# Kernel tuning notes

Measured on AMD Instinct MI355X. Metric: run time of the kernel, lower is better.

The kernel has to match this reference:

```python
import jax, jax.numpy as jnp
import numpy as np

B, S, H, E, K = 4, 4096, 1024, 8, 2
DFF = 4 * H


def setup_inputs() -> dict:
    key = jax.random.key(0)
    ks = jax.random.split(key, 6)
    s_in = 1.0 / np.sqrt(H)
    s_ff = 1.0 / np.sqrt(DFF)
    return {
        "x": jax.random.normal(ks[0], (B, S, H), dtype=jnp.float32),
        "router_w": jax.random.normal(ks[1], (E, H), dtype=jnp.float32) * s_in,
        "router_b": jnp.zeros((E,), dtype=jnp.float32),
        "fc1_w": jax.random.normal(ks[2], (E, DFF, H), dtype=jnp.float32) * s_in,
        "fc1_b": jnp.zeros((E, DFF), dtype=jnp.float32),
        "fc2_w": jax.random.normal(ks[3], (E, H, DFF), dtype=jnp.float32) * s_ff,
        "fc2_b": jnp.zeros((E, H), dtype=jnp.float32),
    }


def reference(x, router_w, router_b, fc1_w, fc1_b, fc2_w, fc2_b):
    b, s, h = x.shape
    e = router_w.shape[0]
    k = K
    # Router: [B,S,E]
    logits = jnp.einsum("bsh,eh->bse", x, router_w) + router_b
    top_v, top_i = jax.lax.top_k(logits, k)            # [B,S,K]
    probs = jax.nn.softmax(top_v, axis=-1)             # softmax over top-k logits
    # Combine weights per expert [B,S,E]; top-k indices are distinct per token,
    # so summing one-hot*prob over k matches the original's gather-of-first-match.
    combine = jnp.sum(jax.nn.one_hot(top_i, e, dtype=x.dtype) * probs[..., None], axis=-2)
    xf = x.reshape(-1, h)            # [T,H], T = B*S
    cf = combine.reshape(-1, e)      # [T,E]
    out = jnp.zeros_like(xf)
    for ei in range(e):              # fixed small loop over experts
        hdn = jax.nn.relu(xf @ fc1_w[ei].T + fc1_b[ei])   # [T,4H]
        y = hdn @ fc2_w[ei].T + fc2_b[ei]                 # [T,H]
        out = out + cf[:, ei:ei + 1] * y                  # zero weight == not routed
    return out.reshape(b, s, h)
```

## Files before the change

### kernel.cpp

```cpp
#include <hip/hip_runtime.h>
#include <stdint.h>

#define T_TOKENS 16384
#define H_DIM 1024
#define E_NUM 8
#define DFF_DIM 4096

#define BMT 128
#define BNT 128
#define BKT 64
#define MT_CAP 264
#define PAD_ROWS (MT_CAP * BMT)
#define NCHUNK 4
#define MT_PER_CHUNK (MT_CAP / NCHUNK)
#define CHUNK_ROWS (MT_PER_CHUNK * BMT)

#define WS_COUNTS     0
#define WS_CURSOR     32
#define WS_OFFS       64
#define WS_SLOT_TOK   256
#define WS_SLOT_W     135424
#define WS_EIDX       270592
#define WS_EW         401664
#define WS_WC1        532736
#define WS_WC2        67641600
#define WS_XB         134750464
#define WS_HDN        168304896
#define WS_REQUIRED   237510912UL
#define WS_SMALL_ZERO 270592

typedef __attribute__((ext_vector_type(8))) short short8;
typedef __attribute__((ext_vector_type(4))) float f32x4;

__device__ __forceinline__ unsigned short f2bf(float f) {
  union { float f; unsigned int u; } v; v.f = f;
  unsigned int r = v.u + 0x7FFFu + ((v.u >> 16) & 1u);
  return (unsigned short)(r >> 16);
}

__device__ __forceinline__ void load_lds16(const void* g, void* l) {
  __builtin_amdgcn_global_load_lds(
      (const __attribute__((address_space(1))) void*)g,
      (__attribute__((address_space(3))) void*)l, 16, 0, 0);
}

__global__ void convert_weights(const float* __restrict__ w1,
                                const float* __restrict__ w2,
                                unsigned short* __restrict__ wc1,
                                unsigned short* __restrict__ wc2) {
  int i = blockIdx.x * blockDim.x + threadIdx.x;
  const float4* s1 = (const float4*)w1;
  const float4* s2 = (const float4*)w2;
  float4 a = s1[i];
  float4 b = s2[i];
  ushort4 ua, ub;
  ua.x = f2bf(a.x); ua.y = f2bf(a.y); ua.z = f2bf(a.z); ua.w = f2bf(a.w);
  ub.x = f2bf(b.x); ub.y = f2bf(b.y); ub.z = f2bf(b.z); ub.w = f2bf(b.w);
  ((ushort4*)wc1)[i] = ua;
  ((ushort4*)wc2)[i] = ub;
}

__global__ __launch_bounds__(256) void router_kernel(
    const float* __restrict__ x, const float* __restrict__ rw,
    const float* __restrict__ rb, unsigned short* __restrict__ xb,
    int* __restrict__ eidx, float* __restrict__ ew) {
  __shared__ float4 rws[E_NUM * 256];
  const int tid = threadIdx.x;
#pragma unroll
  for (int k = 0; k < 8; ++k) rws[k * 256 + tid] = ((const float4*)rw)[k * 256 + tid];
  __syncthreads();

  const int wave = tid >> 6;
  const int lane = tid & 63;
#pragma unroll
  for (int i = 0; i < 4; ++i) {
    const int t = blockIdx.x * 16 + wave * 4 + i;
    const float4* xrow = (const float4*)(x + (size_t)t * H_DIM);
    float4 xv[4];
#pragma unroll
    for (int j = 0; j < 4; ++j) xv[j] = xrow[j * 64 + lane];

    ushort4* xbrow = (ushort4*)(xb + (size_t)t * H_DIM);
#pragma unroll
    for (int j = 0; j < 4; ++j) {
      ushort4 o;
      o.x = f2bf(xv[j].x); o.y = f2bf(xv[j].y);
      o.z = f2bf(xv[j].z); o.w = f2bf(xv[j].w);
      xbrow[j * 64 + lane] = o;
    }

    float s[E_NUM];
#pragma unroll
    for (int e = 0; e < E_NUM; ++e) {
      float a = 0.f;
#pragma unroll
      for (int j = 0; j < 4; ++j) {
        float4 wv = rws[e * 256 + j * 64 + lane];
        a += xv[j].x * wv.x + xv[j].y * wv.y + xv[j].z * wv.z + xv[j].w * wv.w;
      }
      s[e] = a;
    }
#pragma unroll
    for (int off = 32; off; off >>= 1) {
#pragma unroll
      for (int e = 0; e < E_NUM; ++e) s[e] += __shfl_xor(s[e], off);
    }
    if (lane == 0) {
      float lg[E_NUM];
#pragma unroll
      for (int e = 0; e < E_NUM; ++e) lg[e] = s[e] + rb[e];
      int i0 = 0; float m0 = lg[0];
#pragma unroll
      for (int e = 1; e < E_NUM; ++e)
        if (lg[e] > m0) { m0 = lg[e]; i0 = e; }
      int i1 = -1; float m1 = -3.4e38f;
#pragma unroll
      for (int e = 0; e < E_NUM; ++e)
        if (e != i0 && lg[e] > m1) { m1 = lg[e]; i1 = e; }
      float e1 = expf(m1 - m0);
      float denom = 1.f + e1;
      ((int2*)eidx)[t] = make_int2(i0, i1);
      ((float2*)ew)[t] = make_float2(1.f / denom, e1 / denom);
    }
  }
}

__global__ __launch_bounds__(1024) void count_kernel(const int* __restrict__ eidx,
                                                     int* __restrict__ counts,
                                                     int* __restrict__ offs,
                                                     int* __restrict__ cursor) {
  __shared__ int hist[E_NUM];
  const int tid = threadIdx.x;
  const int lane = tid & 63;
  if (tid < E_NUM) hist[tid] = 0;
  __syncthreads();
  int c[E_NUM];
#pragma unroll
  for (int e = 0; e < E_NUM; ++e) c[e] = 0;
  const int4* p = (const int4*)eidx;
#pragma unroll
  for (int i = 0; i < 8; ++i) {
    int4 v = p[i * 1024 + tid];
#pragma unroll
    for (int e = 0; e < E_NUM; ++e)
      c[e] += (v.x == e) + (v.y == e) + (v.z == e) + (v.w == e);
  }
#pragma unroll
  for (int off = 32; off; off >>= 1) {
#pragma unroll
    for (int e = 0; e < E_NUM; ++e) c[e] += __shfl_xor(c[e], off);
  }
  if (lane == 0) {
#pragma unroll
    for (int e = 0; e < E_NUM; ++e) atomicAdd(&hist[e], c[e]);
  }
  __syncthreads();
  if (tid == 0) {
    int acc = 0;
    offs[0] = 0;
#pragma unroll
    for (int e = 0; e < E_NUM; ++e) {
      counts[e] = hist[e];
      cursor[e] = 0;
      acc += ((hist[e] + BMT - 1) / BMT) * BMT;
      offs[e + 1] = acc;
    }
  }
}

__global__ __launch_bounds__(1024) void scatter_kernel(
    const int* __restrict__ eidx, const float* __restrict__ ew,
    const int* __restrict__ offs, int* __restrict__ cursor,
    int* __restrict__ slot_token, float* __restrict__ slot_w) {
  __shared__ int wcnt[16][E_NUM];
  __shared__ int wpre[16][E_NUM];
  __shared__ int bbase[E_NUM];
  __shared__ int soffs[E_NUM];
  const int tid = threadIdx.x, w = tid >> 6, lane = tid & 63;
  const int t = blockIdx.x * 1024 + tid;
  const int2 epair = ((const int2*)eidx)[t];
  const float2 wpair = ((const float2*)ew)[t];
  const int e0 = epair.x, e1 = epair.y;
  const unsigned long long lt = (1ULL << lane) - 1ULL;
  if (tid < E_NUM) soffs[tid] = offs[tid];
  int r0 = 0, r1 = 0;
#pragma unroll
  for (int e = 0; e < E_NUM; ++e) {
    unsigned long long m0 = __ballot(e0 == e);
    unsigned long long m1 = __ballot(e1 == e);
    int c0 = __popcll(m0);
    if (e0 == e) r0 = __popcll(m0 & lt);
    if (e1 == e) r1 = c0 + __popcll(m1 & lt);
    if (lane == 0) wcnt[w][e] = c0 + __popcll(m1);
  }
  __syncthreads();
  if (tid < E_NUM) {
    int run = 0;
#pragma unroll
    for (int w2 = 0; w2 < 16; ++w2) {
      wpre[w2][tid] = run;
      run += wcnt[w2][tid];
    }
    bbase[tid] = atomicAdd(&cursor[tid], run);
  }
  __syncthreads();
  const int s0 = soffs[e0] + bbase[e0] + wpre[w][e0] + r0;
  slot_token[s0] = t;
  slot_w[s0] = wpair.x;
  const int s1 = soffs[e1] + bbase[e1] + wpre[w][e1] + r1;
  slot_token[s1] = t;
  slot_w[s1] = wpair.y;
}

template <int KTOT>
__device__ __forceinline__ void gemm_core(const unsigned short* const* aptr,
                                          const unsigned short* const* bptr,
                                          unsigned short* lA, unsigned short* lB,
                                          f32x4 acc[4][4]) {
  const int tid = threadIdx.x;
  const int w = tid >> 6, lane = tid & 63;
  const int wm = w >> 1, wn = w & 1;
  const int rrow = lane & 15;
  const int rq = lane >> 4;

  for (int ks = 0; ks < KTOT / BKT; ++ks) {
    const int k0 = ks * BKT;
#pragma unroll
    for (int i = 0; i < 4; ++i) {
      load_lds16(aptr[i] + k0, lA + (i * 32 + w * 8) * BKT);
      load_lds16(bptr[i] + k0, lB + (i * 32 + w * 8) * BKT);
    }
    __syncthreads();
#pragma unroll
    for (int kk = 0; kk < 2; ++kk) {
      short8 af[4], bfr[4];
#pragma unroll
      for (int mi = 0; mi < 4; ++mi)
        af[mi] = *(const short8*)(lA + (wm * 64 + mi * 16 + rrow) * BKT + kk * 32 + rq * 8);
#pragma unroll
      for (int ni = 0; ni < 4; ++ni)
        bfr[ni] = *(const short8*)(lB + (wn * 64 + ni * 16 + rrow) * BKT + kk * 32 + rq * 8);
#pragma unroll
      for (int mi = 0; mi < 4; ++mi)
#pragma unroll
        for (int ni = 0; ni < 4; ++ni)
          acc[mi][ni] = __builtin_amdgcn_mfma_f32_16x16x32_bf16(af[mi], bfr[ni], acc[mi][ni], 0, 0, 0);
    }
    __syncthreads();
  }
}

__global__ __launch_bounds__(256, 2) void fc1_kernel(
    const unsigned short* __restrict__ xb, const unsigned short* __restrict__ wc1,
    const float* __restrict__ fc1_b, const int* __restrict__ offs,
    const int* __restrict__ counts, const int* __restrict__ slot_token,
    unsigned short* __restrict__ hdn, int chunk) {
  __shared__ unsigned short sA[BMT * BKT];
  __shared__ unsigned short sB[BNT * BKT];
  const int mt = chunk * MT_PER_CHUNK + blockIdx.y;
  const int row0 = mt * BMT;
  if (row0 >= offs[E_NUM]) return;
  int e = 0;
#pragma unroll
  for (int i = 1; i < E_NUM; ++i) e = (row0 >= offs[i]) ? i : e;
  const int n0 = blockIdx.x * BNT;

  f32x4 acc[4][4];
  f32x4 zf = {0.f, 0.f, 0.f, 0.f};
#pragma unroll
  for (int mi = 0; mi < 4; ++mi)
#pragma unroll
    for (int ni = 0; ni < 4; ++ni) acc[mi][ni] = zf;

  const int w = threadIdx.x >> 6;
  const int lane = threadIdx.x & 63;
  const int srow = w * 8 + (lane >> 3);
  const int scol = (lane & 7) * 8;
  const unsigned short* Bm = wc1 + (size_t)e * DFF_DIM * H_DIM + (size_t)n0 * H_DIM;
  const unsigned short* aptr[4];
  const unsigned short* bptr[4];
#pragma unroll
  for (int i = 0; i < 4; ++i) {
    const int r = i * 32 + srow;
    const int tok = slot_token[row0 + r];
    aptr[i] = xb + (size_t)tok * H_DIM + scol;
    bptr[i] = Bm + (size_t)r * H_DIM + scol;
  }
  gemm_core<H_DIM>(aptr, bptr, sA, sB, acc);

  const int wm = w >> 1, wn = w & 1;
  const int rrow = lane & 15, rq = lane >> 4;
  const int cnt = counts[e];
  const int lbase = row0 - offs[e];
  const int hrow0 = row0 - chunk * CHUNK_ROWS;
#pragma unroll
  for (int mi = 0; mi < 4; ++mi) {
#pragma unroll
    for (int j = 0; j < 4; ++j) {
      const int rit = wm * 64 + mi * 16 + rq * 4 + j;
      if (lbase + rit >= cnt) continue;
      unsigned short* hrow = hdn + (size_t)(hrow0 + rit) * DFF_DIM;
#pragma unroll
      for (int ni = 0; ni < 4; ++ni) {
        const int n = n0 + wn * 64 + ni * 16 + rrow;
        float v = acc[mi][ni][j] + fc1_b[e * DFF_DIM + n];
        v = v > 0.f ? v : 0.f;
        hrow[n] = f2bf(v);
      }
    }
  }
}

__global__ __launch_bounds__(256, 2) void fc2_kernel(
    const unsigned short* __restrict__ hdn, const unsigned short* __restrict__ wc2,
    const float* __restrict__ fc2_b, const int* __restrict__ offs,
    const int* __restrict__ counts, const int* __restrict__ slot_token,
    const float* __restrict__ slot_w, float* __restrict__ out, int chunk) {
  __shared__ unsigned short sA[BMT * BKT];
  __shared__ unsigned short sB[BNT * BKT];
  const int mt = chunk * MT_PER_CHUNK + blockIdx.y;
  const int row0 = mt * BMT;
  if (row0 >= offs[E_NUM]) return;
  int e = 0;
#pragma unroll
  for (int i = 1; i < E_NUM; ++i) e = (row0 >= offs[i]) ? i : e;
  const int n0 = blockIdx.x * BNT;

  f32x4 acc[4][4];
  f32x4 zf = {0.f, 0.f, 0.f, 0.f};
#pragma unroll
  for (int mi = 0; mi < 4; ++mi)
#pragma unroll
    for (int ni = 0; ni < 4; ++ni) acc[mi][ni] = zf;

  const int w = threadIdx.x >> 6;
  const int lane = threadIdx.x & 63;
  const int srow = w * 8 + (lane >> 3);
  const int scol = (lane & 7) * 8;
  const unsigned short* A = hdn + (size_t)(blockIdx.y * BMT) * DFF_DIM;
  const unsigned short* Bm = wc2 + (size_t)e * H_DIM * DFF_DIM + (size_t)n0 * DFF_DIM;
  const unsigned short* aptr[4];
  const unsigned short* bptr[4];
#pragma unroll
  for (int i = 0; i < 4; ++i) {
    const int r = i * 32 + srow;
    aptr[i] = A + (size_t)r * DFF_DIM + scol;
    bptr[i] = Bm + (size_t)r * DFF_DIM + scol;
  }
  gemm_core<DFF_DIM>(aptr, bptr, sA, sB, acc);

  const int wm = w >> 1, wn = w & 1;
  const int rrow = lane & 15, rq = lane >> 4;
  const int cnt = counts[e];
#pragma unroll
  for (int mi = 0; mi < 4; ++mi) {
#pragma unroll
    for (int j = 0; j < 4; ++j) {
      const int rit = wm * 64 + mi * 16 + rq * 4 + j;
      const int gr = row0 + rit;
      if (gr - offs[e] >= cnt) continue;
      const int tok = slot_token[gr];
      const float wgt = slot_w[gr];
      float* orow = out + (size_t)tok * H_DIM;
#pragma unroll
      for (int ni = 0; ni < 4; ++ni) {
        const int h = n0 + wn * 64 + ni * 16 + rrow;
        float v = (acc[mi][ni][j] + fc2_b[e * H_DIM + h]) * wgt;
        atomicAdd(orow + h, v);
      }
    }
  }
}

extern "C" void kernel_launch(void* const* d_in, const int* in_sizes, int n_in,
                              void* d_out, int out_size, void* d_ws, size_t ws_size,
                              hipStream_t stream) {
  const float* x        = (const float*)d_in[0];
  const float* router_w = (const float*)d_in[1];
  const float* router_b = (const float*)d_in[2];
  const float* fc1_w    = (const float*)d_in[3];
  const float* fc1_b    = (const float*)d_in[4];
  const float* fc2_w    = (const float*)d_in[5];
  const float* fc2_b    = (const float*)d_in[6];
  float* out = (float*)d_out;

  char* ws = (char*)d_ws;
  int* counts            = (int*)(ws + WS_COUNTS);
  int* cursor            = (int*)(ws + WS_CURSOR);
  int* offs              = (int*)(ws + WS_OFFS);
  int* slot_token        = (int*)(ws + WS_SLOT_TOK);
  float* slot_w          = (float*)(ws + WS_SLOT_W);
  int* eidx              = (int*)(ws + WS_EIDX);
  float* ew              = (float*)(ws + WS_EW);
  unsigned short* wc1    = (unsigned short*)(ws + WS_WC1);
  unsigned short* wc2    = (unsigned short*)(ws + WS_WC2);
  unsigned short* xb     = (unsigned short*)(ws + WS_XB);
  unsigned short* hdn    = (unsigned short*)(ws + WS_HDN);

  hipMemsetAsync(d_out, 0, (size_t)T_TOKENS * H_DIM * sizeof(float), stream);
  if (ws_size < WS_REQUIRED) return;
  hipMemsetAsync(ws, 0, WS_SMALL_ZERO, stream);

  convert_weights<<<32768, 256, 0, stream>>>(fc1_w, fc2_w, wc1, wc2);
  router_kernel<<<T_TOKENS / 16, 256, 0, stream>>>(x, router_w, router_b, xb, eidx, ew);
  count_kernel<<<1, 1024, 0, stream>>>(eidx, counts, offs, cursor);
  scatter_kernel<<<T_TOKENS / 1024, 1024, 0, stream>>>(eidx, ew, offs, cursor, slot_token, slot_w);

  for (int c = 0; c < NCHUNK; ++c) {
    fc1_kernel<<<dim3(DFF_DIM / BNT, MT_PER_CHUNK), 256, 0, stream>>>(
        xb, wc1, fc1_b, offs, counts, slot_token, hdn, c);
    fc2_kernel<<<dim3(H_DIM / BNT, MT_PER_CHUNK), 256, 0, stream>>>(
        hdn, wc2, fc2_b, offs, counts, slot_token, slot_w, out, c);
  }
}
```

Baseline: 1.143 ms.

## Replace fc2 atomic scatter with bf16 slot outputs and a gather combine kernel

```diff
diff --git a/kernel.cpp b/kernel.cpp
--- a/kernel.cpp
+++ b/kernel.cpp
@@ -8,10 +8,9 @@
 
 #define BMT 128
 #define BNT 128
-#define BKT 64
 #define MT_CAP 264
 #define PAD_ROWS (MT_CAP * BMT)
-#define NCHUNK 4
+#define NCHUNK 8
 #define MT_PER_CHUNK (MT_CAP / NCHUNK)
 #define CHUNK_ROWS (MT_PER_CHUNK * BMT)
 
@@ -19,14 +18,15 @@
 #define WS_CURSOR     32
 #define WS_OFFS       64
 #define WS_SLOT_TOK   256
-#define WS_SLOT_W     135424
 #define WS_EIDX       270592
 #define WS_EW         401664
-#define WS_WC1        532736
-#define WS_WC2        67641600
-#define WS_XB         134750464
-#define WS_HDN        168304896
-#define WS_REQUIRED   237510912UL
+#define WS_TOKSLOT    532736
+#define WS_WC1        663808
+#define WS_WC2        67772672
+#define WS_XB         134881536
+#define WS_HDN        168435968
+#define WS_Y          203038976
+#define WS_REQUIRED   272244992UL
 #define WS_SMALL_ZERO 270592
 
 typedef __attribute__((ext_vector_type(8))) short short8;
@@ -36,6 +36,11 @@
   union { float f; unsigned int u; } v; v.f = f;
   unsigned int r = v.u + 0x7FFFu + ((v.u >> 16) & 1u);
   return (unsigned short)(r >> 16);
+}
+
+__device__ __forceinline__ float bf2f(unsigned short b) {
+  union { unsigned int u; float f; } v; v.u = ((unsigned int)b) << 16;
+  return v.f;
 }
 
 __device__ __forceinline__ void load_lds16(const void* g, void* l) {
@@ -169,9 +174,9 @@
 }
 
 __global__ __launch_bounds__(1024) void scatter_kernel(
-    const int* __restrict__ eidx, const float* __restrict__ ew,
-    const int* __restrict__ offs, int* __restrict__ cursor,
-    int* __restrict__ slot_token, float* __restrict__ slot_w) {
+    const int* __restrict__ eidx, const int* __restrict__ offs,
+    int* __restrict__ cursor, int* __restrict__ slot_token,
+    int* __restrict__ tokslot) {
   __shared__ int wcnt[16][E_NUM];
   __shared__ int wpre[16][E_NUM];
   __shared__ int bbase[E_NUM];
@@ -179,7 +184,6 @@
   const int tid = threadIdx.x, w = tid >> 6, lane = tid & 63;
   const int t = blockIdx.x * 1024 + tid;
   const int2 epair = ((const int2*)eidx)[t];
-  const float2 wpair = ((const float2*)ew)[t];
   const int e0 = epair.x, e1 = epair.y;
   const unsigned long long lt = (1ULL << lane) - 1ULL;
   if (tid < E_NUM) soffs[tid] = offs[tid];
@@ -205,14 +209,13 @@
   }
   __syncthreads();
   const int s0 = soffs[e0] + bbase[e0] + wpre[w][e0] + r0;
+  const int s1 = soffs[e1] + bbase[e1] + wpre[w][e1] + r1;
   slot_token[s0] = t;
-  slot_w[s0] = wpair.x;
-  const int s1 = soffs[e1] + bbase[e1] + wpre[w][e1] + r1;
   slot_token[s1] = t;
-  slot_w[s1] = wpair.y;
-}
-
-template <int KTOT>
+  ((int2*)tokslot)[t] = make_int2(s0, s1);
+}
+
+template <int KTOT, int BK, int NLD>
 __device__ __forceinline__ void gemm_core(const unsigned short* const* aptr,
                                           const unsigned short* const* bptr,
                                           unsigned short* lA, unsigned short* lB,
@@ -223,23 +226,23 @@
   const int rrow = lane & 15;
   const int rq = lane >> 4;
 
-  for (int ks = 0; ks < KTOT / BKT; ++ks) {
-    const int k0 = ks * BKT;
-#pragma unroll
-    for (int i = 0; i < 4; ++i) {
-      load_lds16(aptr[i] + k0, lA + (i * 32 + w * 8) * BKT);
-      load_lds16(bptr[i] + k0, lB + (i * 32 + w * 8) * BKT);
+  for (int ks = 0; ks < KTOT / BK; ++ks) {
+    const int k0 = ks * BK;
+#pragma unroll
+    for (int i = 0; i < NLD; ++i) {
+      load_lds16(aptr[i] + k0, lA + i * 2048 + w * 512);
+      load_lds16(bptr[i] + k0, lB + i * 2048 + w * 512);
     }
     __syncthreads();
 #pragma unroll
-    for (int kk = 0; kk < 2; ++kk) {
+    for (int kk = 0; kk < BK / 32; ++kk) {
       short8 af[4], bfr[4];
 #pragma unroll
       for (int mi = 0; mi < 4; ++mi)
-        af[mi] = *(const short8*)(lA + (wm * 64 + mi * 16 + rrow) * BKT + kk * 32 + rq * 8);
+        af[mi] = *(const short8*)(lA + (wm * 64 + mi * 16 + rrow) * BK + kk * 32 + rq * 8);
 #pragma unroll
       for (int ni = 0; ni < 4; ++ni)
-        bfr[ni] = *(const short8*)(lB + (wn * 64 + ni * 16 + rrow) * BKT + kk * 32 + rq * 8);
+        bfr[ni] = *(const short8*)(lB + (wn * 64 + ni * 16 + rrow) * BK + kk * 32 + rq * 8);
 #pragma unroll
       for (int mi = 0; mi < 4; ++mi)
 #pragma unroll
@@ -255,8 +258,8 @@
     const float* __restrict__ fc1_b, const int* __restrict__ offs,
     const int* __restrict__ counts, const int* __restrict__ slot_token,
     unsigned short* __restrict__ hdn, int chunk) {
-  __shared__ unsigned short sA[BMT * BKT];
-  __shared__ unsigned short sB[BNT * BKT];
+  __shared__ unsigned short sA[BMT * 64];
+  __shared__ unsigned short sB[BNT * 64];
   const int mt = chunk * MT_PER_CHUNK + blockIdx.y;
   const int row0 = mt * BMT;
   if (row0 >= offs[E_NUM]) return;
@@ -272,10 +275,9 @@
 #pragma unroll
     for (int ni = 0; ni < 4; ++ni) acc[mi][ni] = zf;
 
-  const int w = threadIdx.x >> 6;
-  const int lane = threadIdx.x & 63;
-  const int srow = w * 8 + (lane >> 3);
-  const int scol = (lane & 7) * 8;
+  const int tid = threadIdx.x;
+  const int srow = tid >> 3;
+  const int scol = (tid & 7) * 8;
   const unsigned short* Bm = wc1 + (size_t)e * DFF_DIM * H_DIM + (size_t)n0 * H_DIM;
   const unsigned short* aptr[4];
   const unsigned short* bptr[4];
@@ -286,8 +288,10 @@
     aptr[i] = xb + (size_t)tok * H_DIM + scol;
     bptr[i] = Bm + (size_t)r * H_DIM + scol;
   }
-  gemm_core<H_DIM>(aptr, bptr, sA, sB, acc);
-
+  gemm_core<H_DIM, 64, 4>(aptr, bptr, sA, sB, acc);
+
+  const int w = tid >> 6;
+  const int lane = tid & 63;
   const int wm = w >> 1, wn = w & 1;
   const int rrow = lane & 15, rq = lane >> 4;
   const int cnt = counts[e];
@@ -314,17 +318,17 @@
 __global__ __launch_bounds__(256, 2) void fc2_kernel(
     const unsigned short* __restrict__ hdn, const unsigned short* __restrict__ wc2,
     const float* __restrict__ fc2_b, const int* __restrict__ offs,
-    const int* __restrict__ counts, const int* __restrict__ slot_token,
-    const float* __restrict__ slot_w, float* __restrict__ out, int chunk) {
-  __shared__ unsigned short sA[BMT * BKT];
-  __shared__ unsigned short sB[BNT * BKT];
-  const int mt = chunk * MT_PER_CHUNK + blockIdx.y;
+    const int* __restrict__ counts, unsigned short* __restrict__ y, int chunk) {
+  __shared__ unsigned short sA[BMT * 128];
+  __shared__ unsigned short sB[BNT * 128];
+  const int mt_local = blockIdx.x >> 3;
+  const int mt = chunk * MT_PER_CHUNK + mt_local;
   const int row0 = mt * BMT;
   if (row0 >= offs[E_NUM]) return;
   int e = 0;
 #pragma unroll
   for (int i = 1; i < E_NUM; ++i) e = (row0 >= offs[i]) ? i : e;
-  const int n0 = blockIdx.x * BNT;
+  const int n0 = (blockIdx.x & 7) * BNT;
 
   f32x4 acc[4][4];
   f32x4 zf = {0.f, 0.f, 0.f, 0.f};
@@ -333,42 +337,65 @@
 #pragma unroll
     for (int ni = 0; ni < 4; ++ni) acc[mi][ni] = zf;
 
-  const int w = threadIdx.x >> 6;
-  const int lane = threadIdx.x & 63;
-  const int srow = w * 8 + (lane >> 3);
-  const int scol = (lane & 7) * 8;
-  const unsigned short* A = hdn + (size_t)(blockIdx.y * BMT) * DFF_DIM;
+  const int tid = threadIdx.x;
+  const int srow = tid >> 4;
+  const int scol = (tid & 15) * 8;
+  const unsigned short* A = hdn + (size_t)(mt_local * BMT) * DFF_DIM;
   const unsigned short* Bm = wc2 + (size_t)e * H_DIM * DFF_DIM + (size_t)n0 * DFF_DIM;
-  const unsigned short* aptr[4];
-  const unsigned short* bptr[4];
-#pragma unroll
-  for (int i = 0; i < 4; ++i) {
-    const int r = i * 32 + srow;
+  const unsigned short* aptr[8];
+  const unsigned short* bptr[8];
+#pragma unroll
+  for (int i = 0; i < 8; ++i) {
+    const int r = i * 16 + srow;
     aptr[i] = A + (size_t)r * DFF_DIM + scol;
     bptr[i] = Bm + (size_t)r * DFF_DIM + scol;
   }
-  gemm_core<DFF_DIM>(aptr, bptr, sA, sB, acc);
-
+  gemm_core<DFF_DIM, 128, 8>(aptr, bptr, sA, sB, acc);
+
+  const int w = tid >> 6;
+  const int lane = tid & 63;
   const int wm = w >> 1, wn = w & 1;
   const int rrow = lane & 15, rq = lane >> 4;
   const int cnt = counts[e];
+  const int lbase = row0 - offs[e];
 #pragma unroll
   for (int mi = 0; mi < 4; ++mi) {
 #pragma unroll
     for (int j = 0; j < 4; ++j) {
       const int rit = wm * 64 + mi * 16 + rq * 4 + j;
-      const int gr = row0 + rit;
-      if (gr - offs[e] >= cnt) continue;
-      const int tok = slot_token[gr];
-      const float wgt = slot_w[gr];
-      float* orow = out + (size_t)tok * H_DIM;
+      if (lbase + rit >= cnt) continue;
+      unsigned short* yrow = y + (size_t)(row0 + rit) * H_DIM;
 #pragma unroll
       for (int ni = 0; ni < 4; ++ni) {
         const int h = n0 + wn * 64 + ni * 16 + rrow;
-        float v = (acc[mi][ni][j] + fc2_b[e * H_DIM + h]) * wgt;
-        atomicAdd(orow + h, v);
+        yrow[h] = f2bf(acc[mi][ni][j] + fc2_b[e * H_DIM + h]);
       }
     }
+  }
+}
+
+__global__ __launch_bounds__(256) void combine_kernel(
+    const unsigned short* __restrict__ y, const int* __restrict__ tokslot,
+    const float* __restrict__ ew, float* __restrict__ out) {
+  const int wave = threadIdx.x >> 6;
+  const int lane = threadIdx.x & 63;
+  const int t = blockIdx.x * 4 + wave;
+  const int2 sl = ((const int2*)tokslot)[t];
+  const float2 wp = ((const float2*)ew)[t];
+  const ushort4* y0 = (const ushort4*)(y + (size_t)sl.x * H_DIM);
+  const ushort4* y1 = (const ushort4*)(y + (size_t)sl.y * H_DIM);
+  float4* orow = (float4*)(out + (size_t)t * H_DIM);
+#pragma unroll
+  for (int j = 0; j < 4; ++j) {
+    const int idx = j * 64 + lane;
+    ushort4 a = y0[idx];
+    ushort4 b = y1[idx];
+    float4 r;
+    r.x = wp.x * bf2f(a.x) + wp.y * bf2f(b.x);
+    r.y = wp.x * bf2f(a.y) + wp.y * bf2f(b.y);
+    r.z = wp.x * bf2f(a.z) + wp.y * bf2f(b.z);
+    r.w = wp.x * bf2f(a.w) + wp.y * bf2f(b.w);
+    orow[idx] = r;
   }
 }
 
@@ -389,27 +416,31 @@
   int* cursor            = (int*)(ws + WS_CURSOR);
   int* offs              = (int*)(ws + WS_OFFS);
   int* slot_token        = (int*)(ws + WS_SLOT_TOK);
-  float* slot_w          = (float*)(ws + WS_SLOT_W);
   int* eidx              = (int*)(ws + WS_EIDX);
   float* ew              = (float*)(ws + WS_EW);
+  int* tokslot           = (int*)(ws + WS_TOKSLOT);
   unsigned short* wc1    = (unsigned short*)(ws + WS_WC1);
   unsigned short* wc2    = (unsigned short*)(ws + WS_WC2);
   unsigned short* xb     = (unsigned short*)(ws + WS_XB);
   unsigned short* hdn    = (unsigned short*)(ws + WS_HDN);
-
-  hipMemsetAsync(d_out, 0, (size_t)T_TOKENS * H_DIM * sizeof(float), stream);
-  if (ws_size < WS_REQUIRED) return;
+  unsigned short* y      = (unsigned short*)(ws + WS_Y);
+
+  if (ws_size < WS_REQUIRED) {
+    hipMemsetAsync(d_out, 0, (size_t)T_TOKENS * H_DIM * sizeof(float), stream);
+    return;
+  }
   hipMemsetAsync(ws, 0, WS_SMALL_ZERO, stream);
 
   convert_weights<<<32768, 256, 0, stream>>>(fc1_w, fc2_w, wc1, wc2);
   router_kernel<<<T_TOKENS / 16, 256, 0, stream>>>(x, router_w, router_b, xb, eidx, ew);
   count_kernel<<<1, 1024, 0, stream>>>(eidx, counts, offs, cursor);
-  scatter_kernel<<<T_TOKENS / 1024, 1024, 0, stream>>>(eidx, ew, offs, cursor, slot_token, slot_w);
+  scatter_kernel<<<T_TOKENS / 1024, 1024, 0, stream>>>(eidx, offs, cursor, slot_token, tokslot);
 
   for (int c = 0; c < NCHUNK; ++c) {
     fc1_kernel<<<dim3(DFF_DIM / BNT, MT_PER_CHUNK), 256, 0, stream>>>(
         xb, wc1, fc1_b, offs, counts, slot_token, hdn, c);
-    fc2_kernel<<<dim3(H_DIM / BNT, MT_PER_CHUNK), 256, 0, stream>>>(
-        hdn, wc2, fc2_b, offs, counts, slot_token, slot_w, out, c);
-  }
-}
+    fc2_kernel<<<E_NUM * MT_PER_CHUNK, 256, 0, stream>>>(
+        hdn, wc2, fc2_b, offs, counts, y, c);
+  }
+  combine_kernel<<<T_TOKENS / 4, 256, 0, stream>>>(y, tokslot, ew, out);
+}
```

Result: slower. 1.629 ms (+42.5%).

## Replace fc2 atomic accumulation with direct stores plus bf16 side buffer

Applied to the files above, without the earlier changes.

```diff
diff --git a/kernel.cpp b/kernel.cpp
--- a/kernel.cpp
+++ b/kernel.cpp
@@ -26,7 +26,8 @@
 #define WS_WC2        67641600
 #define WS_XB         134750464
 #define WS_HDN        168304896
-#define WS_REQUIRED   237510912UL
+#define WS_OUTK1      237510912
+#define WS_REQUIRED   271065344UL
 #define WS_SMALL_ZERO 270592
 
 typedef __attribute__((ext_vector_type(8))) short short8;
@@ -36,6 +37,11 @@
   union { float f; unsigned int u; } v; v.f = f;
   unsigned int r = v.u + 0x7FFFu + ((v.u >> 16) & 1u);
   return (unsigned short)(r >> 16);
+}
+
+__device__ __forceinline__ float bf2f(unsigned short b) {
+  union { unsigned int u; float f; } v; v.u = ((unsigned int)b) << 16;
+  return v.f;
 }
 
 __device__ __forceinline__ void load_lds16(const void* g, void* l) {
@@ -205,10 +211,10 @@
   }
   __syncthreads();
   const int s0 = soffs[e0] + bbase[e0] + wpre[w][e0] + r0;
+  const int s1 = soffs[e1] + bbase[e1] + wpre[w][e1] + r1;
   slot_token[s0] = t;
   slot_w[s0] = wpair.x;
-  const int s1 = soffs[e1] + bbase[e1] + wpre[w][e1] + r1;
-  slot_token[s1] = t;
+  slot_token[s1] = t | (int)0x80000000;
   slot_w[s1] = wpair.y;
 }
 
@@ -227,8 +233,8 @@
     const int k0 = ks * BKT;
 #pragma unroll
     for (int i = 0; i < 4; ++i) {
-      load_lds16(aptr[i] + k0, lA + (i * 32 + w * 8) * BKT);
-      load_lds16(bptr[i] + k0, lB + (i * 32 + w * 8) * BKT);
+      load_lds16(aptr[i] + k0, lA + i * 2048 + w * 512);
+      load_lds16(bptr[i] + k0, lB + i * 2048 + w * 512);
     }
     __syncthreads();
 #pragma unroll
@@ -272,22 +278,23 @@
 #pragma unroll
     for (int ni = 0; ni < 4; ++ni) acc[mi][ni] = zf;
 
-  const int w = threadIdx.x >> 6;
-  const int lane = threadIdx.x & 63;
-  const int srow = w * 8 + (lane >> 3);
-  const int scol = (lane & 7) * 8;
+  const int tid = threadIdx.x;
+  const int srow = tid >> 3;
+  const int scol = (tid & 7) * 8;
   const unsigned short* Bm = wc1 + (size_t)e * DFF_DIM * H_DIM + (size_t)n0 * H_DIM;
   const unsigned short* aptr[4];
   const unsigned short* bptr[4];
 #pragma unroll
   for (int i = 0; i < 4; ++i) {
     const int r = i * 32 + srow;
-    const int tok = slot_token[row0 + r];
+    const int tok = slot_token[row0 + r] & 0x7FFFFFFF;
     aptr[i] = xb + (size_t)tok * H_DIM + scol;
     bptr[i] = Bm + (size_t)r * H_DIM + scol;
   }
   gemm_core<H_DIM>(aptr, bptr, sA, sB, acc);
 
+  const int w = tid >> 6;
+  const int lane = tid & 63;
   const int wm = w >> 1, wn = w & 1;
   const int rrow = lane & 15, rq = lane >> 4;
   const int cnt = counts[e];
@@ -315,16 +322,22 @@
     const unsigned short* __restrict__ hdn, const unsigned short* __restrict__ wc2,
     const float* __restrict__ fc2_b, const int* __restrict__ offs,
     const int* __restrict__ counts, const int* __restrict__ slot_token,
-    const float* __restrict__ slot_w, float* __restrict__ out, int chunk) {
+    const float* __restrict__ slot_w, float* __restrict__ out,
+    unsigned short* __restrict__ outk1, int chunk) {
   __shared__ unsigned short sA[BMT * BKT];
   __shared__ unsigned short sB[BNT * BKT];
-  const int mt = chunk * MT_PER_CHUNK + blockIdx.y;
+  const int id = blockIdx.x;
+  const int xcd = id & 7, j = id >> 3;
+  int ml, nt;
+  if (j < 64) { ml = xcd * 8 + (j & 7); nt = j >> 3; }
+  else        { ml = 64 + (j & 1);      nt = xcd;    }
+  const int mt = chunk * MT_PER_CHUNK + ml;
   const int row0 = mt * BMT;
   if (row0 >= offs[E_NUM]) return;
   int e = 0;
 #pragma unroll
   for (int i = 1; i < E_NUM; ++i) e = (row0 >= offs[i]) ? i : e;
-  const int n0 = blockIdx.x * BNT;
+  const int n0 = nt * BNT;
 
   f32x4 acc[4][4];
   f32x4 zf = {0.f, 0.f, 0.f, 0.f};
@@ -333,11 +346,10 @@
 #pragma unroll
     for (int ni = 0; ni < 4; ++ni) acc[mi][ni] = zf;
 
-  const int w = threadIdx.x >> 6;
-  const int lane = threadIdx.x & 63;
-  const int srow = w * 8 + (lane >> 3);
-  const int scol = (lane & 7) * 8;
-  const unsigned short* A = hdn + (size_t)(blockIdx.y * BMT) * DFF_DIM;
+  const int tid = threadIdx.x;
+  const int srow = tid >> 3;
+  const int scol = (tid & 7) * 8;
+  const unsigned short* A = hdn + (size_t)(ml * BMT) * DFF_DIM;
   const unsigned short* Bm = wc2 + (size_t)e * H_DIM * DFF_DIM + (size_t)n0 * DFF_DIM;
   const unsigned short* aptr[4];
   const unsigned short* bptr[4];
@@ -349,26 +361,47 @@
   }
   gemm_core<DFF_DIM>(aptr, bptr, sA, sB, acc);
 
+  const int w = tid >> 6;
+  const int lane = tid & 63;
   const int wm = w >> 1, wn = w & 1;
   const int rrow = lane & 15, rq = lane >> 4;
   const int cnt = counts[e];
+  const int lbase = row0 - offs[e];
 #pragma unroll
   for (int mi = 0; mi < 4; ++mi) {
 #pragma unroll
-    for (int j = 0; j < 4; ++j) {
-      const int rit = wm * 64 + mi * 16 + rq * 4 + j;
+    for (int j2 = 0; j2 < 4; ++j2) {
+      const int rit = wm * 64 + mi * 16 + rq * 4 + j2;
+      if (lbase + rit >= cnt) continue;
       const int gr = row0 + rit;
-      if (gr - offs[e] >= cnt) continue;
-      const int tok = slot_token[gr];
+      const int st = slot_token[gr];
+      const int tok = st & 0x7FFFFFFF;
       const float wgt = slot_w[gr];
-      float* orow = out + (size_t)tok * H_DIM;
 #pragma unroll
       for (int ni = 0; ni < 4; ++ni) {
         const int h = n0 + wn * 64 + ni * 16 + rrow;
-        float v = (acc[mi][ni][j] + fc2_b[e * H_DIM + h]) * wgt;
-        atomicAdd(orow + h, v);
+        const float v = (acc[mi][ni][j2] + fc2_b[e * H_DIM + h]) * wgt;
+        if (st >= 0) out[(size_t)tok * H_DIM + h] = v;
+        else         outk1[(size_t)tok * H_DIM + h] = f2bf(v);
       }
     }
+  }
+}
+
+__global__ __launch_bounds__(256) void add_kernel(
+    float* __restrict__ out, const unsigned short* __restrict__ outk1) {
+  const int wave = threadIdx.x >> 6;
+  const int lane = threadIdx.x & 63;
+  const int t = blockIdx.x * 4 + wave;
+  float4* orow = (float4*)(out + (size_t)t * H_DIM);
+  const ushort4* krow = (const ushort4*)(outk1 + (size_t)t * H_DIM);
+#pragma unroll
+  for (int j = 0; j < 4; ++j) {
+    const int idx = j * 64 + lane;
+    float4 a = orow[idx];
+    ushort4 b = krow[idx];
+    a.x += bf2f(b.x); a.y += bf2f(b.y); a.z += bf2f(b.z); a.w += bf2f(b.w);
+    orow[idx] = a;
   }
 }
 
@@ -396,9 +429,12 @@
   unsigned short* wc2    = (unsigned short*)(ws + WS_WC2);
   unsigned short* xb     = (unsigned short*)(ws + WS_XB);
   unsigned short* hdn    = (unsigned short*)(ws + WS_HDN);
-
-  hipMemsetAsync(d_out, 0, (size_t)T_TOKENS * H_DIM * sizeof(float), stream);
-  if (ws_size < WS_REQUIRED) return;
+  unsigned short* outk1  = (unsigned short*)(ws + WS_OUTK1);
+
+  if (ws_size < WS_REQUIRED) {
+    hipMemsetAsync(d_out, 0, (size_t)T_TOKENS * H_DIM * sizeof(float), stream);
+    return;
+  }
   hipMemsetAsync(ws, 0, WS_SMALL_ZERO, stream);
 
   convert_weights<<<32768, 256, 0, stream>>>(fc1_w, fc2_w, wc1, wc2);
@@ -409,7 +445,8 @@
   for (int c = 0; c < NCHUNK; ++c) {
     fc1_kernel<<<dim3(DFF_DIM / BNT, MT_PER_CHUNK), 256, 0, stream>>>(
         xb, wc1, fc1_b, offs, counts, slot_token, hdn, c);
-    fc2_kernel<<<dim3(H_DIM / BNT, MT_PER_CHUNK), 256, 0, stream>>>(
-        hdn, wc2, fc2_b, offs, counts, slot_token, slot_w, out, c);
-  }
-}
+    fc2_kernel<<<E_NUM * MT_PER_CHUNK, 256, 0, stream>>>(
+        hdn, wc2, fc2_b, offs, counts, slot_token, slot_w, out, outk1, c);
+  }
+  add_kernel<<<T_TOKENS / 4, 256, 0, stream>>>(out, outk1);
+}
```

Measured after the change: 1.044 ms. 1.1x faster.
